# Performance work log

Hardware: AMD Instinct MI355X
Metric: run time of the kernel (lower is better)

Reference implementation:

```python
import jax, jax.numpy as jnp
import numpy as np

DISCOUNT_FACTOR = 0.99
ADVANTAGE_LAMBDA = 0.95
LAMBD_GRAD_SCALE = 0.5


def setup_inputs() -> dict:
    key = jax.random.key(0)
    k1, k2, k3 = jax.random.split(key, 3)
    B, T, D = 4096, 2048, 1
    values = jax.random.normal(k1, (B, T + 1, D), dtype=jnp.float32)
    rewards = jax.random.normal(k2, (B, T, D), dtype=jnp.float32)
    # binary terminal flags (float, as in the torch module: used as (1 - dones))
    dones = (jax.random.uniform(k3, (B, T, D)) < 0.02).astype(jnp.float32)
    raw_gamma = jnp.zeros((1,), dtype=jnp.float32)
    raw_lambd = jnp.zeros((T,), dtype=jnp.float32)
    return {
        "values": values,
        "rewards": rewards,
        "dones": dones,
        "raw_gamma": raw_gamma,
        "raw_lambd": raw_lambd,
        "start_idx": 0,
        "end_idx": T,
    }


def reference(values, rewards, dones, raw_gamma, raw_lambd, start_idx, end_idx):
    # dynamic gamma / lambda (sigmoid-reparameterized around the base values)
    gamma = DISCOUNT_FACTOR + (1.0 - DISCOUNT_FACTOR) * (2.0 * jax.nn.sigmoid(raw_gamma) - 1.0)
    dyn_lambd = ADVANTAGE_LAMBDA + (1.0 - ADVANTAGE_LAMBDA) * (2.0 * jax.nn.sigmoid(raw_lambd) - 1.0)
    # GradScaler(scale=0.5): forward identity, gradient scaled by 0.5
    lambd = LAMBD_GRAD_SCALE * dyn_lambd + jax.lax.stop_gradient((1.0 - LAMBD_GRAD_SCALE) * dyn_lambd)
    g = gamma[0]
    td_l = lambd[start_idx:end_idx]                      # [T]

    # time-major views for the reverse-time scan
    r_tm = jnp.moveaxis(rewards, 1, 0)                   # [T, B, D]
    d_tm = jnp.moveaxis(dones, 1, 0)                     # [T, B, D]
    vn_tm = jnp.moveaxis(values[:, 1:, :], 1, 0)         # [T, B, D] = values[t+1]

    def step(carry, x):
        sum_r, lam_ret = carry
        r, d, vn, l = x
        cont = g * (1.0 - d)
        # torch computes sum_rewards under no_grad -> stop_gradient here
        new_sum = jax.lax.stop_gradient(r + cont * (l * sum_r))
        new_lam = r + cont * ((1.0 - l) * vn + l * lam_ret)
        return (new_sum, new_lam), (new_sum, new_lam)

    init = (jnp.zeros_like(values[:, -1, :]), values[:, -1, :])
    _, (sums_tm, lams_tm) = jax.lax.scan(step, init, (r_tm, d_tm, vn_tm, td_l), reverse=True)

    lambda_returns = jnp.concatenate(
        [jnp.moveaxis(lams_tm, 0, 1), values[:, -1:, :]], axis=1
    )                                                    # [B, T+1, D]
    sum_rewards = jnp.moveaxis(sums_tm, 0, 1)            # [B, T, D] (== torch sum_rewards[:, :-1])
    return lambda_returns, sum_rewards
```

## Files before the change

### kernel.cpp

```cpp
#include <hip/hip_runtime.h>


struct Aff { float aL, aS, b; };

__device__ inline Aff compose(const Aff& L, const Aff& R) {
    Aff o;
    o.aL = fmaf(L.b, R.aL, L.aL);
    o.aS = fmaf(L.b, R.aS, L.aS);
    o.b  = L.b * R.b;
    return o;
}

__global__ __launch_bounds__(256)
void td_scan_kernel(const float* __restrict__ values,
                    const float* __restrict__ rewards,
                    const float* __restrict__ dones,
                    const float* __restrict__ raw_gamma,
                    const float* __restrict__ raw_lambd,
                    const int*   __restrict__ start_idx_p,
                    float* __restrict__ out,
                    int B, int T)
{
    const int b    = blockIdx.x;
    const int tid  = threadIdx.x;
    const int lane = tid & 63;
    const int wave = tid >> 6;
    const int nwaves = blockDim.x >> 6;

    __shared__ float s_wAL[8], s_wAS[8], s_wB[8];
    __shared__ float s_cL[9], s_cS[9];

    const float g = 0.98f + 0.02f / (1.0f + __expf(-raw_gamma[0]));
    const int start = start_idx_p[0];

    const float* vrow = values  + (size_t)b * (T + 1);
    const float* rrow = rewards + (size_t)b * T;
    const float* drow = dones   + (size_t)b * T;
    float* lam_out = out + (size_t)b * (T + 1);
    float* sum_out = out + (size_t)B * (T + 1) + (size_t)b * T;

    if (tid == 0) lam_out[T] = vrow[T];

    float carryL = vrow[T];
    float carryS = 0.0f;

    const int P = (T + blockDim.x - 1) / blockDim.x;
    for (int p = P - 1; p >= 0; --p) {
        const int t = p * blockDim.x + tid;

        Aff m;
        if (t < T) {
            const float r  = rrow[t];
            const float d  = drow[t];
            const float vn = vrow[t + 1];
            const float l  = 0.9f + 0.1f / (1.0f + __expf(-raw_lambd[start + t]));
            const float cont = g * (1.0f - d);
            m.b  = cont * l;
            m.aL = fmaf(cont * (1.0f - l), vn, r);
            m.aS = r;
        } else {
            m.aL = 0.0f; m.aS = 0.0f; m.b = 1.0f;
        }

        Aff S = m;
        #pragma unroll
        for (int dlt = 1; dlt < 64; dlt <<= 1) {
            Aff oth;
            oth.aL = __shfl_down(S.aL, dlt, 64);
            oth.aS = __shfl_down(S.aS, dlt, 64);
            oth.b  = __shfl_down(S.b,  dlt, 64);
            if (lane + dlt < 64) S = compose(S, oth);
        }

        if (lane == 0) { s_wAL[wave] = S.aL; s_wAS[wave] = S.aS; s_wB[wave] = S.b; }
        __syncthreads();

        if (tid == 0) {
            float cL = carryL, cS = carryS;
            for (int w = nwaves - 1; w >= 0; --w) {
                s_cL[w] = cL; s_cS[w] = cS;
                const float wb = s_wB[w];
                cL = fmaf(wb, cL, s_wAL[w]);
                cS = fmaf(wb, cS, s_wAS[w]);
            }
            s_cL[nwaves] = cL; s_cS[nwaves] = cS;
        }
        __syncthreads();

        const float cwL = s_cL[wave];
        const float cwS = s_cS[wave];
        const float ncL = s_cL[nwaves];
        const float ncS = s_cS[nwaves];
        __syncthreads();

        if (t < T) {
            lam_out[t] = fmaf(S.b, cwL, S.aL);
            sum_out[t] = fmaf(S.b, cwS, S.aS);
        }
        carryL = ncL;
        carryS = ncS;
    }
}

extern "C" void kernel_launch(void* const* d_in, const int* in_sizes, int n_in,
                              void* d_out, int out_size, void* d_ws, size_t ws_size,
                              hipStream_t stream) {
    const float* values    = (const float*)d_in[0];
    const float* rewards   = (const float*)d_in[1];
    const float* dones     = (const float*)d_in[2];
    const float* raw_gamma = (const float*)d_in[3];
    const float* raw_lambd = (const float*)d_in[4];
    const int*   start_idx = (const int*)d_in[5];
    float* out = (float*)d_out;

    const int n_values  = in_sizes[0];
    const int n_rewards = in_sizes[1];
    const int B = n_values - n_rewards;
    const int T = n_rewards / B;

    td_scan_kernel<<<B, 256, 0, stream>>>(values, rewards, dones, raw_gamma,
                                          raw_lambd, start_idx, out, B, T);
}
```

Measured before the change: 162.7 us.

## Single-pass scan with 4 elements per thread and precomputed lambda

```diff
diff --git a/kernel.cpp b/kernel.cpp
--- a/kernel.cpp
+++ b/kernel.cpp
@@ -11,13 +11,19 @@
     return o;
 }
 
-__global__ __launch_bounds__(256)
+__global__ void lam_precompute(const float* __restrict__ raw_lambd,
+                               const int* __restrict__ start_p,
+                               float* __restrict__ lam, int T) {
+    int t = blockIdx.x * blockDim.x + threadIdx.x;
+    if (t < T) lam[t] = 0.9f + 0.1f / (1.0f + __expf(-raw_lambd[start_p[0] + t]));
+}
+
+__global__ __launch_bounds__(512)
 void td_scan_kernel(const float* __restrict__ values,
                     const float* __restrict__ rewards,
                     const float* __restrict__ dones,
                     const float* __restrict__ raw_gamma,
-                    const float* __restrict__ raw_lambd,
-                    const int*   __restrict__ start_idx_p,
+                    const float* __restrict__ lam_arr,
                     float* __restrict__ out,
                     int B, int T)
 {
@@ -28,10 +34,10 @@
     const int nwaves = blockDim.x >> 6;
 
     __shared__ float s_wAL[8], s_wAS[8], s_wB[8];
-    __shared__ float s_cL[9], s_cS[9];
+    __shared__ float s_cL[8], s_cS[8];
+    __shared__ float s_vT;
 
     const float g = 0.98f + 0.02f / (1.0f + __expf(-raw_gamma[0]));
-    const int start = start_idx_p[0];
 
     const float* vrow = values  + (size_t)b * (T + 1);
     const float* rrow = rewards + (size_t)b * T;
@@ -39,66 +45,106 @@
     float* lam_out = out + (size_t)b * (T + 1);
     float* sum_out = out + (size_t)B * (T + 1) + (size_t)b * T;
 
-    if (tid == 0) lam_out[T] = vrow[T];
+    const int base = tid * 4;
 
-    float carryL = vrow[T];
-    float carryS = 0.0f;
+    float r[4], d[4], l[4], vn[4];
+    const bool full = (base + 3) < T;
+    if (full) {
+        const float4 r4 = *(const float4*)(rrow + base);
+        const float4 d4 = *(const float4*)(drow + base);
+        const float4 l4 = *(const float4*)(lam_arr + base);
+        r[0]=r4.x; r[1]=r4.y; r[2]=r4.z; r[3]=r4.w;
+        d[0]=d4.x; d[1]=d4.y; d[2]=d4.z; d[3]=d4.w;
+        l[0]=l4.x; l[1]=l4.y; l[2]=l4.z; l[3]=l4.w;
+        vn[0]=vrow[base+1]; vn[1]=vrow[base+2]; vn[2]=vrow[base+3]; vn[3]=vrow[base+4];
+    } else {
+        #pragma unroll
+        for (int k = 0; k < 4; ++k) {
+            const int t = base + k;
+            r[k] = (t < T) ? rrow[t] : 0.0f;
+            d[k] = (t < T) ? drow[t] : 1.0f;
+            l[k] = (t < T) ? lam_arr[t] : 0.0f;
+            vn[k] = (t < T) ? vrow[t + 1] : 0.0f;
+        }
+    }
+    if (tid == 0) {
+        float vT = vrow[T];
+        s_vT = vT;
+        lam_out[T] = vT;
+    }
 
-    const int P = (T + blockDim.x - 1) / blockDim.x;
-    for (int p = P - 1; p >= 0; --p) {
-        const int t = p * blockDim.x + tid;
+    Aff M[4];
+    #pragma unroll
+    for (int k = 0; k < 4; ++k) {
+        const int t = base + k;
+        if (t < T) {
+            const float cont = g * (1.0f - d[k]);
+            M[k].b  = cont * l[k];
+            M[k].aL = fmaf(cont * (1.0f - l[k]), vn[k], r[k]);
+            M[k].aS = r[k];
+        } else {
+            M[k].aL = 0.0f; M[k].aS = 0.0f; M[k].b = 1.0f;
+        }
+    }
+    Aff C = M[3];
+    C = compose(M[2], C);
+    C = compose(M[1], C);
+    C = compose(M[0], C);
 
-        Aff m;
-        if (t < T) {
-            const float r  = rrow[t];
-            const float d  = drow[t];
-            const float vn = vrow[t + 1];
-            const float l  = 0.9f + 0.1f / (1.0f + __expf(-raw_lambd[start + t]));
-            const float cont = g * (1.0f - d);
-            m.b  = cont * l;
-            m.aL = fmaf(cont * (1.0f - l), vn, r);
-            m.aS = r;
-        } else {
-            m.aL = 0.0f; m.aS = 0.0f; m.b = 1.0f;
+    Aff S = C;
+    #pragma unroll
+    for (int dlt = 1; dlt < 64; dlt <<= 1) {
+        Aff oth;
+        oth.aL = __shfl_down(S.aL, dlt, 64);
+        oth.aS = __shfl_down(S.aS, dlt, 64);
+        oth.b  = __shfl_down(S.b,  dlt, 64);
+        if (lane + dlt < 64) S = compose(S, oth);
+    }
+    Aff E;
+    E.aL = __shfl_down(S.aL, 1, 64);
+    E.aS = __shfl_down(S.aS, 1, 64);
+    E.b  = __shfl_down(S.b,  1, 64);
+    if (lane == 63) { E.aL = 0.0f; E.aS = 0.0f; E.b = 1.0f; }
+
+    if (lane == 0) { s_wAL[wave] = S.aL; s_wAS[wave] = S.aS; s_wB[wave] = S.b; }
+    __syncthreads();
+
+    if (tid == 0) {
+        float cL = s_vT, cS = 0.0f;
+        for (int w = nwaves - 1; w >= 0; --w) {
+            s_cL[w] = cL; s_cS[w] = cS;
+            const float wb = s_wB[w];
+            cL = fmaf(wb, cL, s_wAL[w]);
+            cS = fmaf(wb, cS, s_wAS[w]);
         }
+    }
+    __syncthreads();
 
-        Aff S = m;
+    const float cwL = s_cL[wave];
+    const float cwS = s_cS[wave];
+    float xL = fmaf(E.b, cwL, E.aL);
+    float xS = fmaf(E.b, cwS, E.aS);
+
+    float oL[4], oS[4];
+    #pragma unroll
+    for (int k = 3; k >= 0; --k) {
+        xL = fmaf(M[k].b, xL, M[k].aL);
+        xS = fmaf(M[k].b, xS, M[k].aS);
+        oL[k] = xL; oS[k] = xS;
+    }
+
+    if (full) {
+        *(float4*)(sum_out + base) = make_float4(oS[0], oS[1], oS[2], oS[3]);
+        lam_out[base + 0] = oL[0];
+        lam_out[base + 1] = oL[1];
+        lam_out[base + 2] = oL[2];
+        lam_out[base + 3] = oL[3];
+    } else {
         #pragma unroll
-        for (int dlt = 1; dlt < 64; dlt <<= 1) {
-            Aff oth;
-            oth.aL = __shfl_down(S.aL, dlt, 64);
-            oth.aS = __shfl_down(S.aS, dlt, 64);
-            oth.b  = __shfl_down(S.b,  dlt, 64);
-            if (lane + dlt < 64) S = compose(S, oth);
+        for (int k = 0; k < 4; ++k) {
+            const int t = base + k;
+            if (t < T) { lam_out[t] = oL[k]; sum_out[t] = oS[k]; }
         }
-
-        if (lane == 0) { s_wAL[wave] = S.aL; s_wAS[wave] = S.aS; s_wB[wave] = S.b; }
-        __syncthreads();
-
-        if (tid == 0) {
-            float cL = carryL, cS = carryS;
-            for (int w = nwaves - 1; w >= 0; --w) {
-                s_cL[w] = cL; s_cS[w] = cS;
-                const float wb = s_wB[w];
-                cL = fmaf(wb, cL, s_wAL[w]);
-                cS = fmaf(wb, cS, s_wAS[w]);
-            }
-            s_cL[nwaves] = cL; s_cS[nwaves] = cS;
-        }
-        __syncthreads();
-
-        const float cwL = s_cL[wave];
-        const float cwS = s_cS[wave];
-        const float ncL = s_cL[nwaves];
-        const float ncS = s_cS[nwaves];
-        __syncthreads();
-
-        if (t < T) {
-            lam_out[t] = fmaf(S.b, cwL, S.aL);
-            sum_out[t] = fmaf(S.b, cwS, S.aS);
-        }
-        carryL = ncL;
-        carryS = ncS;
     }
 }
 
@@ -112,12 +158,14 @@
     const float* raw_lambd = (const float*)d_in[4];
     const int*   start_idx = (const int*)d_in[5];
     float* out = (float*)d_out;
+    float* lam_arr = (float*)d_ws;
 
     const int n_values  = in_sizes[0];
     const int n_rewards = in_sizes[1];
     const int B = n_values - n_rewards;
     const int T = n_rewards / B;
 
-    td_scan_kernel<<<B, 256, 0, stream>>>(values, rewards, dones, raw_gamma,
-                                          raw_lambd, start_idx, out, B, T);
+    lam_precompute<<<(T + 255) / 256, 256, 0, stream>>>(raw_lambd, start_idx, lam_arr, T);
+    td_scan_kernel<<<B, 512, 0, stream>>>(values, rewards, dones, raw_gamma,
+                                          lam_arr, out, B, T);
 }
```

Result: faster. 153.9 us (-5.4%).

## Scan each row in one wavefront with 32 elements per lane in registers

Applied to the files above, without the earlier changes.

```diff
diff --git a/kernel.cpp b/kernel.cpp
--- a/kernel.cpp
+++ b/kernel.cpp
@@ -1,5 +1,10 @@
 #include <hip/hip_runtime.h>
 
+
+#define TPB 256
+#define EPT 32
+
+typedef float v4f __attribute__((ext_vector_type(4)));
 
 struct Aff { float aL, aS, b; };
 
@@ -11,94 +16,181 @@
     return o;
 }
 
-__global__ __launch_bounds__(256)
+__global__ void precompute_kernel(const float* __restrict__ raw_gamma,
+                                  const float* __restrict__ raw_lambd,
+                                  const int* __restrict__ start_p,
+                                  float* __restrict__ lam, int T) {
+    int t = blockIdx.x * blockDim.x + threadIdx.x;
+    if (t < T) lam[t] = 0.9f + 0.1f / (1.0f + __expf(-raw_lambd[start_p[0] + t]));
+    if (t == 0) lam[T] = 0.98f + 0.02f / (1.0f + __expf(-raw_gamma[0]));
+}
+
+__global__ __launch_bounds__(TPB)
 void td_scan_kernel(const float* __restrict__ values,
                     const float* __restrict__ rewards,
                     const float* __restrict__ dones,
-                    const float* __restrict__ raw_gamma,
-                    const float* __restrict__ raw_lambd,
-                    const int*   __restrict__ start_idx_p,
+                    const float* __restrict__ lam_arr,
                     float* __restrict__ out,
                     int B, int T)
 {
-    const int b    = blockIdx.x;
-    const int tid  = threadIdx.x;
-    const int lane = tid & 63;
-    const int wave = tid >> 6;
-    const int nwaves = blockDim.x >> 6;
-
-    __shared__ float s_wAL[8], s_wAS[8], s_wB[8];
-    __shared__ float s_cL[9], s_cS[9];
-
-    const float g = 0.98f + 0.02f / (1.0f + __expf(-raw_gamma[0]));
-    const int start = start_idx_p[0];
-
-    const float* vrow = values  + (size_t)b * (T + 1);
+    const int lane = threadIdx.x & 63;
+    const int b    = blockIdx.x * (TPB / 64) + (threadIdx.x >> 6);
+    if (b >= B) return;
+
+    const float g = lam_arr[T];
+
+    const size_t rowV = (size_t)b * (T + 1);
     const float* rrow = rewards + (size_t)b * T;
     const float* drow = dones   + (size_t)b * T;
-    float* lam_out = out + (size_t)b * (T + 1);
-    float* sum_out = out + (size_t)B * (T + 1) + (size_t)b * T;
-
-    if (tid == 0) lam_out[T] = vrow[T];
-
-    float carryL = vrow[T];
-    float carryS = 0.0f;
-
-    const int P = (T + blockDim.x - 1) / blockDim.x;
-    for (int p = P - 1; p >= 0; --p) {
-        const int t = p * blockDim.x + tid;
-
-        Aff m;
-        if (t < T) {
-            const float r  = rrow[t];
-            const float d  = drow[t];
-            const float vn = vrow[t + 1];
-            const float l  = 0.9f + 0.1f / (1.0f + __expf(-raw_lambd[start + t]));
-            const float cont = g * (1.0f - d);
-            m.b  = cont * l;
-            m.aL = fmaf(cont * (1.0f - l), vn, r);
-            m.aS = r;
-        } else {
-            m.aL = 0.0f; m.aS = 0.0f; m.b = 1.0f;
+    const int base = lane * EPT;
+
+    v4f R4[8], D4[8], L4[8];
+    #pragma unroll
+    for (int j = 0; j < 8; ++j) {
+        R4[j] = *(const v4f*)(rrow + base + 4 * j);
+        D4[j] = *(const v4f*)(drow + base + 4 * j);
+        L4[j] = *(const v4f*)(lam_arr + base + 4 * j);
+    }
+    const int off = (int)((rowV + 1) & 3);
+    const float* wbase = values + (rowV + 1 - off) + base;
+    float w[36];
+    #pragma unroll
+    for (int j = 0; j < 8; ++j) *(v4f*)(w + 4 * j) = *(const v4f*)(wbase + 4 * j);
+    w[32] = w[33] = w[34] = w[35] = 0.0f;
+    if (off) {
+        const size_t gidx = (rowV + 1 - off) + base + 32;
+        const size_t totalV = (size_t)B * (T + 1);
+        #pragma unroll
+        for (int c = 0; c < 3; ++c)
+            if (gidx + c < totalV) w[32 + c] = values[gidx + c];
+    }
+    const float vT = values[rowV + T];
+
+    float vn[32];
+    switch (off) {
+    case 0: { 
+        #pragma unroll
+        for (int k = 0; k < 32; ++k) vn[k] = w[k];     } break;
+    case 1: { 
+        #pragma unroll
+        for (int k = 0; k < 32; ++k) vn[k] = w[k + 1]; } break;
+    case 2: { 
+        #pragma unroll
+        for (int k = 0; k < 32; ++k) vn[k] = w[k + 2]; } break;
+    default: { 
+        #pragma unroll
+        for (int k = 0; k < 32; ++k) vn[k] = w[k + 3]; } break;
+    }
+
+    float bb[32], aL[32], aS[32];
+    #pragma unroll
+    for (int k = 0; k < 32; ++k) {
+        const float rr = R4[k >> 2][k & 3];
+        const float dd = D4[k >> 2][k & 3];
+        const float ll = L4[k >> 2][k & 3];
+        const float cont = g * (1.0f - dd);
+        bb[k] = cont * ll;
+        aL[k] = fmaf(cont * (1.0f - ll), vn[k], rr);
+        aS[k] = rr;
+    }
+
+    Aff C4[8];
+    #pragma unroll
+    for (int c = 0; c < 8; ++c) {
+        Aff m0 = { aL[4*c+0], aS[4*c+0], bb[4*c+0] };
+        Aff m1 = { aL[4*c+1], aS[4*c+1], bb[4*c+1] };
+        Aff m2 = { aL[4*c+2], aS[4*c+2], bb[4*c+2] };
+        Aff m3 = { aL[4*c+3], aS[4*c+3], bb[4*c+3] };
+        C4[c] = compose(compose(m0, m1), compose(m2, m3));
+    }
+    Aff c2a = compose(C4[0], C4[1]), c2b = compose(C4[2], C4[3]);
+    Aff c2c = compose(C4[4], C4[5]), c2d = compose(C4[6], C4[7]);
+    Aff c3a = compose(c2a, c2b);
+    Aff S_hi = compose(c2c, c2d);
+    Aff C = compose(c3a, S_hi);
+
+    Aff S = C;
+    #pragma unroll
+    for (int dlt = 1; dlt < 64; dlt <<= 1) {
+        Aff o;
+        o.aL = __shfl_down(S.aL, dlt, 64);
+        o.aS = __shfl_down(S.aS, dlt, 64);
+        o.b  = __shfl_down(S.b,  dlt, 64);
+        if (lane + dlt < 64) S = compose(S, o);
+    }
+    Aff E;
+    E.aL = __shfl_down(S.aL, 1, 64);
+    E.aS = __shfl_down(S.aS, 1, 64);
+    E.b  = __shfl_down(S.b,  1, 64);
+    if (lane == 63) { E.aL = 0.0f; E.aS = 0.0f; E.b = 1.0f; }
+
+    float xL = fmaf(E.b, vT, E.aL);
+    float xS = E.aS;
+
+    float xmL = fmaf(S_hi.b, xL, S_hi.aL);
+    float xmS = fmaf(S_hi.b, xS, S_hi.aS);
+    #pragma unroll
+    for (int k = 15; k >= 0; --k) {
+        const int kb = k + 16;
+        xL  = fmaf(bb[kb], xL,  aL[kb]);  xS  = fmaf(bb[kb], xS,  aS[kb]);
+        aL[kb] = xL;  aS[kb] = xS;
+        xmL = fmaf(bb[k],  xmL, aL[k]);   xmS = fmaf(bb[k],  xmS, aS[k]);
+        aL[k] = xmL;  aS[k] = xmS;
+    }
+
+    float* sum_out = out + (size_t)B * (T + 1) + (size_t)b * T + base;
+    #pragma unroll
+    for (int j = 0; j < 8; ++j) {
+        v4f s = { aS[4*j], aS[4*j+1], aS[4*j+2], aS[4*j+3] };
+        *(v4f*)(sum_out + 4 * j) = s;
+    }
+
+    const size_t O = (size_t)b * (T + 1);
+    float* lamrow = out + O;
+    const int sh = (int)((4 - (O & 3)) & 3);
+    float nb0 = __shfl_down(aL[0], 1, 64);
+    float nb1 = __shfl_down(aL[1], 1, 64);
+    float nb2 = __shfl_down(aL[2], 1, 64);
+    if (lane == 63) nb0 = vT;
+
+    float z[32];
+    switch (sh) {
+    case 0: { 
+        #pragma unroll
+        for (int m = 0; m < 32; ++m) z[m] = aL[m];
+        } break;
+    case 1: { 
+        #pragma unroll
+        for (int m = 0; m < 31; ++m) z[m] = aL[m + 1];
+        z[31] = nb0; } break;
+    case 2: { 
+        #pragma unroll
+        for (int m = 0; m < 30; ++m) z[m] = aL[m + 2];
+        z[30] = nb0; z[31] = nb1; } break;
+    default: { 
+        #pragma unroll
+        for (int m = 0; m < 29; ++m) z[m] = aL[m + 3];
+        z[29] = nb0; z[30] = nb1; z[31] = nb2; } break;
+    }
+    #pragma unroll
+    for (int j = 0; j < 8; ++j) {
+        const int t0 = base + sh + 4 * j;
+        if (t0 + 3 <= T) {
+            v4f v = { z[4*j], z[4*j+1], z[4*j+2], z[4*j+3] };
+            *(v4f*)(lamrow + t0) = v;
         }
-
-        Aff S = m;
-        #pragma unroll
-        for (int dlt = 1; dlt < 64; dlt <<= 1) {
-            Aff oth;
-            oth.aL = __shfl_down(S.aL, dlt, 64);
-            oth.aS = __shfl_down(S.aS, dlt, 64);
-            oth.b  = __shfl_down(S.b,  dlt, 64);
-            if (lane + dlt < 64) S = compose(S, oth);
+    }
+    if (lane == 0) {
+        for (int m = 0; m < sh; ++m) lamrow[m] = aL[m];
+    }
+    if (lane == 63) {
+        const int J  = (sh <= 1) ? 8 : 7;
+        const int LC = (33 - sh) & 3;
+        const int firstLocal = sh + 4 * J;
+        for (int m = 0; m < LC; ++m) {
+            const int loc = firstLocal + m;
+            lamrow[base + loc] = (loc < 32) ? aL[loc] : vT;
         }
-
-        if (lane == 0) { s_wAL[wave] = S.aL; s_wAS[wave] = S.aS; s_wB[wave] = S.b; }
-        __syncthreads();
-
-        if (tid == 0) {
-            float cL = carryL, cS = carryS;
-            for (int w = nwaves - 1; w >= 0; --w) {
-                s_cL[w] = cL; s_cS[w] = cS;
-                const float wb = s_wB[w];
-                cL = fmaf(wb, cL, s_wAL[w]);
-                cS = fmaf(wb, cS, s_wAS[w]);
-            }
-            s_cL[nwaves] = cL; s_cS[nwaves] = cS;
-        }
-        __syncthreads();
-
-        const float cwL = s_cL[wave];
-        const float cwS = s_cS[wave];
-        const float ncL = s_cL[nwaves];
-        const float ncS = s_cS[nwaves];
-        __syncthreads();
-
-        if (t < T) {
-            lam_out[t] = fmaf(S.b, cwL, S.aL);
-            sum_out[t] = fmaf(S.b, cwS, S.aS);
-        }
-        carryL = ncL;
-        carryS = ncS;
     }
 }
 
@@ -112,12 +204,16 @@
     const float* raw_lambd = (const float*)d_in[4];
     const int*   start_idx = (const int*)d_in[5];
     float* out = (float*)d_out;
+    float* lam_arr = (float*)d_ws;
 
     const int n_values  = in_sizes[0];
     const int n_rewards = in_sizes[1];
     const int B = n_values - n_rewards;
     const int T = n_rewards / B;
 
-    td_scan_kernel<<<B, 256, 0, stream>>>(values, rewards, dones, raw_gamma,
-                                          raw_lambd, start_idx, out, B, T);
-}
+    precompute_kernel<<<(T + 256) / 256, 256, 0, stream>>>(raw_gamma, raw_lambd,
+                                                           start_idx, lam_arr, T);
+    const int rowsPerBlock = TPB / 64;
+    td_scan_kernel<<<(B + rowsPerBlock - 1) / rowsPerBlock, TPB, 0, stream>>>(
+        values, rewards, dones, lam_arr, out, B, T);
+}
```

After: 168.9 us. +3.8%, slower.
